# Kernel tuning notes

Hardware: AMD Instinct MI355X
Metric: run time of the kernel (lower is better)

Reference implementation:

```python
import jax, jax.numpy as jnp
import numpy as np
import math

B, T, D, H = 2, 2048, 1024, 16
DH = D // H          # 64
NB = DH // 2         # 32 rotary pairs
EPS = 1e-5


def setup_inputs() -> dict:
    key = jax.random.key(0)
    ks = jax.random.split(key, 20)
    x = jax.random.normal(ks[0], (B, T, D), dtype=jnp.float32)
    angles = jax.random.uniform(ks[1], (B, H, T, NB), dtype=jnp.float32) * (2.0 * math.pi)
    cos_a = jnp.cos(angles)
    sin_a = jnp.sin(angles)
    sigma = jax.random.uniform(ks[2], (B, T, H, NB), dtype=jnp.float32)
    causal_mask = jnp.triu(jnp.ones((T, T), dtype=bool), k=1)  # True above diag -> masked
    w = lambda k, i, o: jax.random.normal(k, (i, o), dtype=jnp.float32) * 0.02
    return {
        "x": x, "cos_a": cos_a, "sin_a": sin_a, "sigma": sigma, "causal_mask": causal_mask,
        "ln1_g": jnp.ones((D,), jnp.float32), "ln1_b": jnp.zeros((D,), jnp.float32),
        "wq": w(ks[3], D, D), "bq": jnp.zeros((D,), jnp.float32),
        "wk": w(ks[4], D, D), "bk": jnp.zeros((D,), jnp.float32),
        "wv": w(ks[5], D, D), "bv": jnp.zeros((D,), jnp.float32),
        "wo": w(ks[6], D, D), "bo": jnp.zeros((D,), jnp.float32),
        "ln2_g": jnp.ones((D,), jnp.float32), "ln2_b": jnp.zeros((D,), jnp.float32),
        "w1": w(ks[7], D, 4 * D), "b1": jnp.zeros((4 * D,), jnp.float32),
        "w2": w(ks[8], 4 * D, D), "b2": jnp.zeros((D,), jnp.float32),
    }


def _layer_norm(x, g, b):
    mu = jnp.mean(x, axis=-1, keepdims=True)
    var = jnp.mean(jnp.square(x - mu), axis=-1, keepdims=True)
    return (x - mu) * jax.lax.rsqrt(var + EPS) * g + b


def _apply_rope(q, cos_a, sin_a):
    # q: (B,H,T,DH); rotate even/odd pairs by per-pair angles (B,H,T,NB)
    q1 = q[..., 0::2]
    q2 = q[..., 1::2]
    re = q1 * cos_a - q2 * sin_a
    im = q1 * sin_a + q2 * cos_a
    return jnp.stack([re, im], axis=-1).reshape(q.shape)


def reference(x, cos_a, sin_a, sigma, causal_mask,
              ln1_g, ln1_b, wq, bq, wk, bk, wv, bv, wo, bo,
              ln2_g, ln2_b, w1, b1, w2, b2):
    h = _layer_norm(x, ln1_g, ln1_b)
    Q = (h @ wq + bq).reshape(B, T, H, DH).transpose(0, 2, 1, 3)
    K = (h @ wk + bk).reshape(B, T, H, DH).transpose(0, 2, 1, 3)
    V = (h @ wv + bv).reshape(B, T, H, DH).transpose(0, 2, 1, 3)
    Q = _apply_rope(Q, cos_a, sin_a)
    K = _apply_rope(K, cos_a, sin_a)
    # per-(B,H,T) temperature from mean uncertainty
    temp = 1.0 + jnp.mean(sigma, axis=-1).transpose(0, 2, 1)  # (B,H,T)
    scale = math.sqrt(DH)
    scores = jnp.einsum("bhtd,bhsd->bhts", Q, K) / (scale * temp[..., None])
    scores = jnp.where(causal_mask[None, None], -jnp.inf, scores)
    attn = jax.nn.softmax(scores, axis=-1)
    out = jnp.einsum("bhts,bhsd->bhtd", attn, V)
    out = out.transpose(0, 2, 1, 3).reshape(B, T, D)
    x = x + (out @ wo + bo)
    h2 = _layer_norm(x, ln2_g, ln2_b)
    ffn = jax.nn.gelu(h2 @ w1 + b1, approximate=False) @ w2 + b2
    return x + ffn
```

## Files before the change

kernel.cpp:

```cpp
#include <hip/hip_runtime.h>

typedef unsigned short ushort;
typedef unsigned int uint;

typedef __attribute__((ext_vector_type(8))) short short8;
typedef __attribute__((ext_vector_type(8))) unsigned short ushort8;
typedef __attribute__((ext_vector_type(4))) unsigned short ushort4v;
typedef __attribute__((ext_vector_type(4))) float f32x4;
typedef __attribute__((ext_vector_type(4))) uint uint4v;

#define DEV static __device__ __forceinline__

DEV ushort f2b(float f){
  union { float f; uint u; } v; v.f = f;
  uint u = v.u;
  u += 0x7fffu + ((u >> 16) & 1u);
  return (ushort)(u >> 16);
}
DEV float b2f(ushort h){
  union { uint u; float f; } v; v.u = ((uint)h) << 16;
  return v.f;
}
DEV uint cvt_pk_bf16(float lo, float hi){
  uint r;
  asm("v_cvt_pk_bf16_f32 %0, %1, %2" : "=v"(r) : "v"(lo), "v"(hi));
  return r;
}
DEV ushort f2b1(float f){ return (ushort)cvt_pk_bf16(f, f); }
DEV float exp2v(float x){
  float r;
  asm("v_exp_f32 %0, %1" : "=v"(r) : "v"(x));
  return r;
}
DEV float gelu_f(float x){
  float z = fabsf(x) * 0.70710678118654752f;
  float t = __builtin_amdgcn_rcpf(1.f + 0.3275911f * z);
  float poly = t * (0.254829592f + t * (-0.284496736f + t * (1.421413741f +
               t * (-1.453152027f + t * 1.061405429f))));
  float e = exp2v(-z * z * 1.44269504088896f);
  float erf_abs = 1.f - poly * e;
  float erf_s = copysignf(erf_abs, x);
  return 0.5f * x * (1.f + erf_s);
}

constexpr int Bc = 2, Tc = 2048, Dc = 1024, Hc = 16, DHc = 64, NBc = 32;
constexpr int Rc = Bc * Tc;
constexpr int D4c = 4 * Dc;

__global__ __launch_bounds__(256) void k_transcvt(const float* __restrict__ in,
                                                  ushort* __restrict__ out, int K, int N){
  __shared__ float tile[32][33];
  int n0 = blockIdx.x * 32, k0 = blockIdx.y * 32;
  int c = threadIdx.x & 31, r0 = threadIdx.x >> 5;
#pragma unroll
  for (int i = 0; i < 4; i++){
    int k = r0 + i * 8;
    tile[k][c] = in[(size_t)(k0 + k) * N + n0 + c];
  }
  __syncthreads();
#pragma unroll
  for (int i = 0; i < 4; i++){
    int n = r0 + i * 8;
    out[(size_t)(n0 + n) * K + k0 + c] = f2b(tile[c][n]);
  }
}

__global__ __launch_bounds__(256) void k_ln(const float* __restrict__ x, const float* __restrict__ g,
                                            const float* __restrict__ bb, ushort* __restrict__ out){
  int row = blockIdx.x, tid = threadIdx.x;
  const f32x4* xr = (const f32x4*)(x + (size_t)row * Dc);
  f32x4 v = xr[tid];
  float s  = v.x + v.y + v.z + v.w;
  float ss = v.x*v.x + v.y*v.y + v.z*v.z + v.w*v.w;
#pragma unroll
  for (int off = 32; off > 0; off >>= 1){
    s  += __shfl_xor(s,  off, 64);
    ss += __shfl_xor(ss, off, 64);
  }
  __shared__ float red[2][4];
  int w = tid >> 6;
  if ((tid & 63) == 0){ red[0][w] = s; red[1][w] = ss; }
  __syncthreads();
  s  = red[0][0] + red[0][1] + red[0][2] + red[0][3];
  ss = red[1][0] + red[1][1] + red[1][2] + red[1][3];
  float mu  = s * (1.f / Dc);
  float var = ss * (1.f / Dc) - mu * mu;
  float rs  = rsqrtf(var + 1e-5f);
  f32x4 gv = ((const f32x4*)g)[tid];
  f32x4 bv = ((const f32x4*)bb)[tid];
  ushort4v o;
  o.x = f2b((v.x - mu) * rs * gv.x + bv.x);
  o.y = f2b((v.y - mu) * rs * gv.y + bv.y);
  o.z = f2b((v.z - mu) * rs * gv.z + bv.z);
  o.w = f2b((v.w - mu) * rs * gv.w + bv.w);
  ((ushort4v*)(out + (size_t)row * Dc))[tid] = o;
}

#define GLDS(src, dst) __builtin_amdgcn_global_load_lds( \
    (const __attribute__((address_space(1))) void*)(src), \
    (__attribute__((address_space(3))) void*)(dst), 16, 0, 0)

#define STAGE128(nb_, k0_) do { \
  _Pragma("unroll") \
  for (int i_ = 0; i_ < 4; i_++){ \
    int chunk_ = w * 4 + i_; \
    GLDS(A  + (size_t)(m0 + chunk_ * 8 + rloc) * K + (k0_) + gsrc * 8, &SM[nb_][0][chunk_ * 512]); \
    GLDS(Bt + (size_t)(n0 + chunk_ * 8 + rloc) * K + (k0_) + gsrc * 8, &SM[nb_][1][chunk_ * 512]); \
  } \
} while(0)

#define GEMM_CORE(cb_) do { \
  _Pragma("unroll") \
  for (int ks = 0; ks < 2; ks++){ \
    const int gs = (ks * 4 + lg) ^ l7; \
    short8 aF[4], bF[4]; \
    _Pragma("unroll") \
    for (int mi = 0; mi < 4; mi++) aF[mi] = *(const short8*)&SM[cb_][0][(arow + mi * 16) * 64 + gs * 8]; \
    _Pragma("unroll") \
    for (int ni = 0; ni < 4; ni++) bF[ni] = *(const short8*)&SM[cb_][1][(brow + ni * 16) * 64 + gs * 8]; \
    _Pragma("unroll") \
    for (int mi = 0; mi < 4; mi++) \
      _Pragma("unroll") \
      for (int ni = 0; ni < 4; ni++) \
        acc[mi][ni] = __builtin_amdgcn_mfma_f32_16x16x32_bf16(aF[mi], bF[ni], acc[mi][ni], 0, 0, 0); \
  } \
} while(0)

template<int OUT_BF16, int ACT_GELU, int HAS_RES>
__global__ __launch_bounds__(256) void k_gemm(const ushort* __restrict__ A, const ushort* __restrict__ Bt,
                                              const float* __restrict__ bias, const float* __restrict__ resid,
                                              void* __restrict__ Cout, int M, int N, int K){
  __shared__ ushort SM[2][2][8192];
  const int tid = threadIdx.x;
  const int m0 = blockIdx.y * 128, n0 = blockIdx.x * 128;
  const int w = tid >> 6, lane = tid & 63;
  const int wr = w >> 1, wc = w & 1;
  const int la15 = lane & 15, lg = lane >> 4, l7 = lane & 7;
  const int rloc = lane >> 3, gsrc = (lane & 7) ^ rloc;

  f32x4 acc[4][4];
#pragma unroll
  for (int i = 0; i < 4; i++)
#pragma unroll
    for (int j = 0; j < 4; j++) acc[i][j] = f32x4{0.f, 0.f, 0.f, 0.f};

  const int arow = wr * 64 + la15;
  const int brow = wc * 64 + la15;

  STAGE128(0, 0);
  __syncthreads();
  const int NT = K >> 6;
  for (int t = 0; t < NT; t++){
    const int cb = t & 1;
    if (t + 1 < NT) STAGE128(cb ^ 1, (t + 1) << 6);
    GEMM_CORE(cb);
    __syncthreads();
  }

  if (OUT_BF16){
    ushort* Cs = &SM[0][0][0];
#pragma unroll
    for (int mi = 0; mi < 4; mi++)
#pragma unroll
      for (int ni = 0; ni < 4; ni++){
        int ccl = wc * 64 + ni * 16 + la15;
        float bv = bias[n0 + ccl];
        f32x4 a4 = acc[mi][ni];
#pragma unroll
        for (int r = 0; r < 4; r++){
          int rl = wr * 64 + mi * 16 + lg * 4 + r;
          float v = a4[r] + bv;
          if (ACT_GELU) v = gelu_f(v);
          Cs[rl * 136 + ccl] = f2b1(v);
        }
      }
    __syncthreads();
#pragma unroll
    for (int p = 0; p < 8; p++){
      int row = p * 16 + (tid >> 4);
      int col = (tid & 15) * 8;
      ushort8 vv = *(const ushort8*)&Cs[row * 136 + col];
      *(ushort8*)((ushort*)Cout + (size_t)(m0 + row) * N + n0 + col) = vv;
    }
  } else {
#pragma unroll
    for (int mi = 0; mi < 4; mi++)
#pragma unroll
      for (int ni = 0; ni < 4; ni++){
        int cc = n0 + wc * 64 + ni * 16 + la15;
        float bv = bias[cc];
        f32x4 a4 = acc[mi][ni];
#pragma unroll
        for (int r = 0; r < 4; r++){
          int rr = m0 + wr * 64 + mi * 16 + lg * 4 + r;
          float v = a4[r] + bv;
          if (HAS_RES) v += resid[(size_t)rr * N + cc];
          ((float*)Cout)[(size_t)rr * N + cc] = v;
        }
      }
  }
}

__global__ __launch_bounds__(256) void k_gemm_qkv(const ushort* __restrict__ A, const ushort* __restrict__ Bt,
                                                  const float* __restrict__ bq_, const float* __restrict__ bk_,
                                                  const float* __restrict__ bv_, ushort* __restrict__ oq,
                                                  ushort* __restrict__ ok, ushort* __restrict__ ovt, int K){
  __shared__ ushort SM[2][2][8192];
  const int tid = threadIdx.x;
  const int m0 = blockIdx.y * 128, n0 = blockIdx.x * 128;
  const int w = tid >> 6, lane = tid & 63;
  const int wr = w >> 1, wc = w & 1;
  const int la15 = lane & 15, lg = lane >> 4, l7 = lane & 7;
  const int rloc = lane >> 3, gsrc = (lane & 7) ^ rloc;

  f32x4 acc[4][4];
#pragma unroll
  for (int i = 0; i < 4; i++)
#pragma unroll
    for (int j = 0; j < 4; j++) acc[i][j] = f32x4{0.f, 0.f, 0.f, 0.f};

  const int arow = wr * 64 + la15;
  const int brow = wc * 64 + la15;

  STAGE128(0, 0);
  __syncthreads();
  const int NT = K >> 6;
  for (int t = 0; t < NT; t++){
    const int cb = t & 1;
    if (t + 1 < NT) STAGE128(cb ^ 1, (t + 1) << 6);
    GEMM_CORE(cb);
    __syncthreads();
  }

  const int sel = n0 >> 10;
  ushort* Cs = &SM[0][0][0];
  if (sel < 2){
    const float* bias = sel == 0 ? bq_ : bk_;
    ushort* o = sel == 0 ? oq : ok;
#pragma unroll
    for (int mi = 0; mi < 4; mi++)
#pragma unroll
      for (int ni = 0; ni < 4; ni++){
        int ccl = wc * 64 + ni * 16 + la15;
        float bv = bias[(n0 & 1023) + ccl];
        f32x4 a4 = acc[mi][ni];
#pragma unroll
        for (int r = 0; r < 4; r++){
          int rl = wr * 64 + mi * 16 + lg * 4 + r;
          Cs[rl * 136 + ccl] = f2b1(a4[r] + bv);
        }
      }
    __syncthreads();
#pragma unroll
    for (int p = 0; p < 8; p++){
      int row = p * 16 + (tid >> 4);
      int col = (tid & 15) * 8;
      ushort8 vv = *(const ushort8*)&Cs[row * 136 + col];
      *(ushort8*)(o + (size_t)(m0 + row) * Dc + (n0 & 1023) + col) = vv;
    }
  } else {
#pragma unroll
    for (int mi = 0; mi < 4; mi++)
#pragma unroll
      for (int ni = 0; ni < 4; ni++){
        int ccl = wc * 64 + ni * 16 + la15;
        float bv = bv_[(n0 - 2048) + ccl];
        f32x4 a4 = acc[mi][ni];
#pragma unroll
        for (int r = 0; r < 4; r++){
          int rl = wr * 64 + mi * 16 + lg * 4 + r;
          Cs[ccl * 136 + rl] = f2b1(a4[r] + bv);
        }
      }
    __syncthreads();
    const int bb = m0 >> 11, t0 = m0 & 2047;
#pragma unroll
    for (int p = 0; p < 8; p++){
      int nl = p * 16 + (tid >> 4);
      int tl = (tid & 15) * 8;
      ushort8 vv = *(const ushort8*)&Cs[nl * 136 + tl];
      int ng = (n0 - 2048) + nl;
      *(ushort8*)(ovt + ((size_t)(bb * 1024 + ng) << 11) + t0 + tl) = vv;
    }
  }
}

__global__ __launch_bounds__(256) void k_rope(ushort* __restrict__ q, ushort* __restrict__ k,
                                              const float* __restrict__ ca, const float* __restrict__ sa){
  int idx = blockIdx.x * 256 + threadIdx.x;
  int nb = idx & 31;
  int hh = (idx >> 5) & 15;
  int t  = (idx >> 9) & 2047;
  int b  = idx >> 20;
  size_t base = (size_t)(b * Tc + t) * Dc + hh * DHc + nb * 2;
  int ai = ((b * Hc + hh) * Tc + t) * NBc + nb;
  float c = ca[ai], s = sa[ai];
  uint qu = *(const uint*)(q + base);
  float q1 = b2f((ushort)(qu & 0xffff)), q2 = b2f((ushort)(qu >> 16));
  *(uint*)(q + base) = cvt_pk_bf16(q1 * c - q2 * s, q1 * s + q2 * c);
  uint ku = *(const uint*)(k + base);
  float k1 = b2f((ushort)(ku & 0xffff)), k2 = b2f((ushort)(ku >> 16));
  *(uint*)(k + base) = cvt_pk_bf16(k1 * c - k2 * s, k1 * s + k2 * c);
}

__global__ __launch_bounds__(256) void k_iscale(const float* __restrict__ sigma, float* __restrict__ isc){
  int idx = blockIdx.x * 256 + threadIdx.x;
  int hh = idx & 15;
  int t  = (idx >> 4) & 2047;
  int b  = idx >> 15;
  const f32x4* sp = (const f32x4*)(sigma + (size_t)idx * NBc);
  float s = 0.f;
#pragma unroll
  for (int i = 0; i < 8; i++){ f32x4 v = sp[i]; s += v.x + v.y + v.z + v.w; }
  isc[(b * Hc + hh) * Tc + t] = 1.44269504088896f / (8.f * (1.f + s * (1.f / NBc)));
}

__global__ __launch_bounds__(64) void k_attn_mfma(const ushort* __restrict__ qb, const ushort* __restrict__ kb,
                                                  const ushort* __restrict__ vtb, const float* __restrict__ isc,
                                                  ushort* __restrict__ ao){
  const int bid = blockIdx.x;
  const int bh = bid & 31, b = bh >> 4, h = bh & 15;
  const int qt = 63 - (bid >> 5);
  const int lane = threadIdx.x;
  const int la15 = lane & 15, lg = lane >> 4, l7 = lane & 7;
  const int q0w = qt * 32;
  const int kprm = ((la15 >> 2) << 3) + (la15 & 3);

  short8 qf[2][2];
  float iscv[2];
#pragma unroll
  for (int sub = 0; sub < 2; sub++){
    int qg = q0w + sub * 16 + la15;
    size_t rb = (size_t)(b * Tc + qg) * Dc + h * DHc;
    qf[sub][0] = *(const short8*)(qb + rb + lg * 8);
    qf[sub][1] = *(const short8*)(qb + rb + 32 + lg * 8);
    iscv[sub] = isc[bh * Tc + qg];
  }

  f32x4 O[2][4];
#pragma unroll
  for (int sub = 0; sub < 2; sub++)
#pragma unroll
    for (int dt = 0; dt < 4; dt++) O[sub][dt] = f32x4{0.f, 0.f, 0.f, 0.f};
  float lacc[2] = {0.f, 0.f};

  const ushort* kbase  = kb + (size_t)b * Tc * Dc + h * DHc;
  const ushort* vtbase = vtb + (size_t)bh * DHc * Tc;
  const int ktmax = q0w + 31;

#define LOADT(KF, VF, kt_) do { \
  _Pragma("unroll") \
  for (int tt_ = 0; tt_ < 4; tt_++){ \
    const ushort* kr_ = kbase + (size_t)((kt_) + kprm + ((tt_ & 1) << 2) + ((tt_ >> 1) << 5)) * Dc + lg * 8; \
    KF[tt_][0] = *(const short8*)kr_; \
    KF[tt_][1] = *(const short8*)(kr_ + 32); \
  } \
  _Pragma("unroll") \
  for (int dd_ = 0; dd_ < 4; dd_++){ \
    const ushort* vr_ = vtbase + (size_t)(dd_ * 16 + la15) * Tc + (kt_) + lg * 8; \
    VF[dd_][0] = *(const short8*)vr_; \
    VF[dd_][1] = *(const short8*)(vr_ + 32); \
  } \
} while(0)

#define COMPUTE(KF, VF, kt_) do { \
  _Pragma("unroll") \
  for (int sub = 0; sub < 2; sub++){ \
    f32x4 s_[4]; \
    _Pragma("unroll") \
    for (int t_ = 0; t_ < 4; t_++){ \
      s_[t_] = f32x4{0.f, 0.f, 0.f, 0.f}; \
      s_[t_] = __builtin_amdgcn_mfma_f32_16x16x32_bf16(KF[t_][0], qf[sub][0], s_[t_], 0, 0, 0); \
      s_[t_] = __builtin_amdgcn_mfma_f32_16x16x32_bf16(KF[t_][1], qf[sub][1], s_[t_], 0, 0, 0); \
    } \
    const int qg_ = q0w + sub * 16 + la15; \
    const float sc_ = iscv[sub]; \
    const bool diag_ = ((kt_) + 63 > q0w + sub * 16); \
    uint up_[4][2]; \
    float lp_ = 0.f; \
    _Pragma("unroll") \
    for (int t_ = 0; t_ < 4; t_++){ \
      _Pragma("unroll") \
      for (int pr_ = 0; pr_ < 2; pr_++){ \
        float e0_ = exp2v(s_[t_][2 * pr_] * sc_); \
        float e1_ = exp2v(s_[t_][2 * pr_ + 1] * sc_); \
        if (diag_){ \
          int kp0_ = (kt_) + ((t_ >> 1) << 5) + lg * 8 + ((t_ & 1) << 2) + 2 * pr_; \
          if (kp0_ > qg_)     e0_ = 0.f; \
          if (kp0_ + 1 > qg_) e1_ = 0.f; \
        } \
        lp_ += e0_ + e1_; \
        up_[t_][pr_] = cvt_pk_bf16(e0_, e1_); \
      } \
    } \
    lacc[sub] += lp_; \
    _Pragma("unroll") \
    for (int kh_ = 0; kh_ < 2; kh_++){ \
      union { uint4v w; short8 s8; } pfr_; \
      pfr_.w[0] = up_[kh_ * 2][0];     pfr_.w[1] = up_[kh_ * 2][1]; \
      pfr_.w[2] = up_[kh_ * 2 + 1][0]; pfr_.w[3] = up_[kh_ * 2 + 1][1]; \
      _Pragma("unroll") \
      for (int dt_ = 0; dt_ < 4; dt_++) \
        O[sub][dt_] = __builtin_amdgcn_mfma_f32_16x16x32_bf16(VF[dt_][kh_], pfr_.s8, O[sub][dt_], 0, 0, 0); \
    } \
  } \
} while(0)

  short8 kfA[4][2], vtfA[4][2], kfB[4][2], vtfB[4][2];
  LOADT(kfA, vtfA, 0);
  for (int kt = 0;; kt += 128){
    if (kt + 64 <= ktmax) LOADT(kfB, vtfB, kt + 64);
    COMPUTE(kfA, vtfA, kt);
    if (kt + 64 > ktmax) break;
    if (kt + 128 <= ktmax) LOADT(kfA, vtfA, kt + 128);
    COMPUTE(kfB, vtfB, kt + 64);
    if (kt + 128 > ktmax) break;
  }

  __shared__ ushort os[2176];
  char* osb = (char*)os;
#pragma unroll
  for (int sub = 0; sub < 2; sub++){
    float lt = lacc[sub];
    lt += __shfl_xor(lt, 16, 64);
    lt += __shfl_xor(lt, 32, 64);
    float inv = 1.f / lt;
#pragma unroll
    for (int dt = 0; dt < 4; dt++)
#pragma unroll
      for (int pr = 0; pr < 2; pr++){
        uint u = cvt_pk_bf16(O[sub][dt][2 * pr] * inv, O[sub][dt][2 * pr + 1] * inv);
        *(uint*)(osb + (sub * 16 + la15) * 136 + (dt * 16 + lg * 4 + pr * 2) * 2) = u;
      }
  }
#pragma unroll
  for (int it = 0; it < 4; it++){
    int ql = it * 8 + (lane >> 3);
    ushort8 v = *(const ushort8*)(osb + ql * 136 + l7 * 16);
    *(ushort8*)(ao + (size_t)(b * Tc + q0w + ql) * Dc + h * DHc + l7 * 8) = v;
  }
}

extern "C" void kernel_launch(void* const* d_in, const int* in_sizes, int n_in,
                              void* d_out, int out_size, void* d_ws, size_t ws_size,
                              hipStream_t stream){
  (void)in_sizes; (void)n_in; (void)out_size; (void)ws_size;
  const float* x    = (const float*)d_in[0];
  const float* cosa = (const float*)d_in[1];
  const float* sina = (const float*)d_in[2];
  const float* sigma= (const float*)d_in[3];
  const float* ln1g = (const float*)d_in[5];
  const float* ln1b = (const float*)d_in[6];
  const float* wq   = (const float*)d_in[7];
  const float* bq   = (const float*)d_in[8];
  const float* wk   = (const float*)d_in[9];
  const float* bk   = (const float*)d_in[10];
  const float* wv   = (const float*)d_in[11];
  const float* bv   = (const float*)d_in[12];
  const float* wo   = (const float*)d_in[13];
  const float* bo   = (const float*)d_in[14];
  const float* ln2g = (const float*)d_in[15];
  const float* ln2b = (const float*)d_in[16];
  const float* w1   = (const float*)d_in[17];
  const float* b1   = (const float*)d_in[18];
  const float* w2   = (const float*)d_in[19];
  const float* b2   = (const float*)d_in[20];
  float* out = (float*)d_out;

  char* ws = (char*)d_ws;
  constexpr size_t MB = 1024 * 1024;
  ushort* wqT  = (ushort*)(ws +  0 * MB);
  ushort* wkT  = (ushort*)(ws +  2 * MB);
  ushort* wvT  = (ushort*)(ws +  4 * MB);
  ushort* woT  = (ushort*)(ws +  6 * MB);
  ushort* w1T  = (ushort*)(ws +  8 * MB);
  ushort* w2T  = (ushort*)(ws + 16 * MB);
  ushort* hb   = (ushort*)(ws + 24 * MB);
  ushort* qbuf = (ushort*)(ws + 32 * MB);
  ushort* kbuf = (ushort*)(ws + 40 * MB);
  ushort* vtb  = (ushort*)(ws + 48 * MB);
  ushort* aob  = (ushort*)(ws + 56 * MB);
  float*  x2   = (float*)(ws + 64 * MB);
  float*  iscp = (float*)(ws + 80 * MB);
  ushort* g1b  = qbuf;

  k_transcvt<<<dim3(Dc / 32, Dc / 32), 256, 0, stream>>>(wq, wqT, Dc, Dc);
  k_transcvt<<<dim3(Dc / 32, Dc / 32), 256, 0, stream>>>(wk, wkT, Dc, Dc);
  k_transcvt<<<dim3(Dc / 32, Dc / 32), 256, 0, stream>>>(wv, wvT, Dc, Dc);
  k_transcvt<<<dim3(Dc / 32, Dc / 32), 256, 0, stream>>>(wo, woT, Dc, Dc);
  k_transcvt<<<dim3(D4c / 32, Dc / 32), 256, 0, stream>>>(w1, w1T, Dc, D4c);
  k_transcvt<<<dim3(Dc / 32, D4c / 32), 256, 0, stream>>>(w2, w2T, D4c, Dc);
  k_ln<<<Rc, 256, 0, stream>>>(x, ln1g, ln1b, hb);
  k_gemm_qkv<<<dim3(3 * Dc / 128, Rc / 128), 256, 0, stream>>>(hb, wqT, bq, bk, bv, qbuf, kbuf, vtb, Dc);
  k_rope<<<(Bc * Tc * Hc * NBc) / 256, 256, 0, stream>>>(qbuf, kbuf, cosa, sina);
  k_iscale<<<(Bc * Tc * Hc) / 256, 256, 0, stream>>>(sigma, iscp);
  k_attn_mfma<<<dim3(2048), 64, 0, stream>>>(qbuf, kbuf, vtb, iscp, aob);
  k_gemm<0, 0, 1><<<dim3(Dc / 128, Rc / 128), 256, 0, stream>>>(aob, woT, bo, x, x2, Rc, Dc, Dc);
  k_ln<<<Rc, 256, 0, stream>>>(x2, ln2g, ln2b, hb);
  k_gemm<1, 1, 0><<<dim3(D4c / 128, Rc / 128), 256, 0, stream>>>(hb, w1T, b1, nullptr, g1b, Rc, D4c, Dc);
  k_gemm<0, 0, 1><<<dim3(Dc / 128, Rc / 128), 256, 0, stream>>>(g1b, w2T, b2, x2, out, Rc, Dc, D4c);
}
```

Baseline: 265.1 us.

## Use a four-stage LDS ring pipeline in GEMMs and prefetch deeper in attention

The GEMM main loop moves from a two-buffer, 64-wide K step to a four-slot LDS ring with a 32-wide K step. Three stages stay in flight, gated by explicit vmcnt waits and raw barriers, and a new XOR swizzle matches the narrower tiles. MFMA blocks in both the GEMM and attention kernels are wrapped in s_setprio so matrix work gets issue priority. The attention loop now prefetches the next K/V tile unconditionally, and its launch bounds change to (64, 1). Both kernels now issue speculative loads past the valid K range, which risks out-of-bounds reads on the final iterations.

```diff
diff --git a/kernel.cpp b/kernel.cpp
--- a/kernel.cpp
+++ b/kernel.cpp
@@ -100,43 +100,63 @@
     (const __attribute__((address_space(1))) void*)(src), \
     (__attribute__((address_space(3))) void*)(dst), 16, 0, 0)
 
-#define STAGE128(nb_, k0_) do { \
+#define STAGE_R(ring_, k0_) do { \
+  GLDS(A  + (size_t)(m0 + grow)      * K + (k0_) + g4 * 8, &SM[ring_][0][w * 512]); \
+  GLDS(A  + (size_t)(m0 + 64 + grow) * K + (k0_) + g4 * 8, &SM[ring_][0][2048 + w * 512]); \
+  GLDS(Bt + (size_t)(n0 + grow)      * K + (k0_) + g4 * 8, &SM[ring_][1][w * 512]); \
+  GLDS(Bt + (size_t)(n0 + 64 + grow) * K + (k0_) + g4 * 8, &SM[ring_][1][2048 + w * 512]); \
+} while(0)
+
+#define CORE_R(cb_) do { \
+  const ushort* As_ = &SM[cb_][0][0]; \
+  const ushort* Bs_ = &SM[cb_][1][0]; \
+  short8 aF[4], bF[4]; \
   _Pragma("unroll") \
-  for (int i_ = 0; i_ < 4; i_++){ \
-    int chunk_ = w * 4 + i_; \
-    GLDS(A  + (size_t)(m0 + chunk_ * 8 + rloc) * K + (k0_) + gsrc * 8, &SM[nb_][0][chunk_ * 512]); \
-    GLDS(Bt + (size_t)(n0 + chunk_ * 8 + rloc) * K + (k0_) + gsrc * 8, &SM[nb_][1][chunk_ * 512]); \
+  for (int mi = 0; mi < 4; mi++){ \
+    int r_ = arow + mi * 16; \
+    aF[mi] = *(const short8*)&As_[r_ * 32 + (lg ^ ((r_ >> 1) & 3)) * 8]; \
   } \
+  _Pragma("unroll") \
+  for (int ni = 0; ni < 4; ni++){ \
+    int r_ = brow + ni * 16; \
+    bF[ni] = *(const short8*)&Bs_[r_ * 32 + (lg ^ ((r_ >> 1) & 3)) * 8]; \
+  } \
+  __builtin_amdgcn_s_setprio(1); \
+  _Pragma("unroll") \
+  for (int mi = 0; mi < 4; mi++) \
+    _Pragma("unroll") \
+    for (int ni = 0; ni < 4; ni++) \
+      acc[mi][ni] = __builtin_amdgcn_mfma_f32_16x16x32_bf16(aF[mi], bF[ni], acc[mi][ni], 0, 0, 0); \
+  __builtin_amdgcn_s_setprio(0); \
 } while(0)
 
-#define GEMM_CORE(cb_) do { \
-  _Pragma("unroll") \
-  for (int ks = 0; ks < 2; ks++){ \
-    const int gs = (ks * 4 + lg) ^ l7; \
-    short8 aF[4], bF[4]; \
-    _Pragma("unroll") \
-    for (int mi = 0; mi < 4; mi++) aF[mi] = *(const short8*)&SM[cb_][0][(arow + mi * 16) * 64 + gs * 8]; \
-    _Pragma("unroll") \
-    for (int ni = 0; ni < 4; ni++) bF[ni] = *(const short8*)&SM[cb_][1][(brow + ni * 16) * 64 + gs * 8]; \
-    _Pragma("unroll") \
-    for (int mi = 0; mi < 4; mi++) \
-      _Pragma("unroll") \
-      for (int ni = 0; ni < 4; ni++) \
-        acc[mi][ni] = __builtin_amdgcn_mfma_f32_16x16x32_bf16(aF[mi], bF[ni], acc[mi][ni], 0, 0, 0); \
+#define RING_LOOP() do { \
+  STAGE_R(0, 0); STAGE_R(1, 32); STAGE_R(2, 64); \
+  asm volatile("s_waitcnt vmcnt(8)" ::: "memory"); \
+  __builtin_amdgcn_s_barrier(); \
+  const int NT_ = K >> 5; \
+  for (int t = 0; t < NT_; t++){ \
+    STAGE_R((t + 3) & 3, (t + 3) << 5); \
+    CORE_R(t & 3); \
+    asm volatile("s_waitcnt vmcnt(8)" ::: "memory"); \
+    __builtin_amdgcn_s_barrier(); \
   } \
+  asm volatile("s_waitcnt vmcnt(0)" ::: "memory"); \
+  __builtin_amdgcn_s_barrier(); \
 } while(0)
 
 template<int OUT_BF16, int ACT_GELU, int HAS_RES>
 __global__ __launch_bounds__(256) void k_gemm(const ushort* __restrict__ A, const ushort* __restrict__ Bt,
                                               const float* __restrict__ bias, const float* __restrict__ resid,
                                               void* __restrict__ Cout, int M, int N, int K){
-  __shared__ ushort SM[2][2][8192];
+  __shared__ ushort SM[4][2][4096];
   const int tid = threadIdx.x;
   const int m0 = blockIdx.y * 128, n0 = blockIdx.x * 128;
   const int w = tid >> 6, lane = tid & 63;
   const int wr = w >> 1, wc = w & 1;
-  const int la15 = lane & 15, lg = lane >> 4, l7 = lane & 7;
-  const int rloc = lane >> 3, gsrc = (lane & 7) ^ rloc;
+  const int la15 = lane & 15, lg = lane >> 4;
+  const int grow = w * 16 + (lane >> 2);
+  const int g4 = (lane & 3) ^ ((lane >> 3) & 3);
 
   f32x4 acc[4][4];
 #pragma unroll
@@ -147,18 +167,10 @@
   const int arow = wr * 64 + la15;
   const int brow = wc * 64 + la15;
 
-  STAGE128(0, 0);
-  __syncthreads();
-  const int NT = K >> 6;
-  for (int t = 0; t < NT; t++){
-    const int cb = t & 1;
-    if (t + 1 < NT) STAGE128(cb ^ 1, (t + 1) << 6);
-    GEMM_CORE(cb);
-    __syncthreads();
-  }
+  RING_LOOP();
 
   if (OUT_BF16){
-    ushort* Cs = &SM[0][0][0];
+    ushort* Cs = (ushort*)SM;
 #pragma unroll
     for (int mi = 0; mi < 4; mi++)
 #pragma unroll
@@ -168,7 +180,7 @@
         f32x4 a4 = acc[mi][ni];
 #pragma unroll
         for (int r = 0; r < 4; r++){
-          int rl = wr * 64 + mi * 16 + lg * 4 + r;
+          int rl = wr * 64 + mi * 16 + (lane >> 4) * 4 + r;
           float v = a4[r] + bv;
           if (ACT_GELU) v = gelu_f(v);
           Cs[rl * 136 + ccl] = f2b1(v);
@@ -192,7 +204,7 @@
         f32x4 a4 = acc[mi][ni];
 #pragma unroll
         for (int r = 0; r < 4; r++){
-          int rr = m0 + wr * 64 + mi * 16 + lg * 4 + r;
+          int rr = m0 + wr * 64 + mi * 16 + (lane >> 4) * 4 + r;
           float v = a4[r] + bv;
           if (HAS_RES) v += resid[(size_t)rr * N + cc];
           ((float*)Cout)[(size_t)rr * N + cc] = v;
@@ -205,13 +217,14 @@
                                                   const float* __restrict__ bq_, const float* __restrict__ bk_,
                                                   const float* __restrict__ bv_, ushort* __restrict__ oq,
                                                   ushort* __restrict__ ok, ushort* __restrict__ ovt, int K){
-  __shared__ ushort SM[2][2][8192];
+  __shared__ ushort SM[4][2][4096];
   const int tid = threadIdx.x;
   const int m0 = blockIdx.y * 128, n0 = blockIdx.x * 128;
   const int w = tid >> 6, lane = tid & 63;
   const int wr = w >> 1, wc = w & 1;
-  const int la15 = lane & 15, lg = lane >> 4, l7 = lane & 7;
-  const int rloc = lane >> 3, gsrc = (lane & 7) ^ rloc;
+  const int la15 = lane & 15, lg = lane >> 4;
+  const int grow = w * 16 + (lane >> 2);
+  const int g4 = (lane & 3) ^ ((lane >> 3) & 3);
 
   f32x4 acc[4][4];
 #pragma unroll
@@ -222,18 +235,10 @@
   const int arow = wr * 64 + la15;
   const int brow = wc * 64 + la15;
 
-  STAGE128(0, 0);
-  __syncthreads();
-  const int NT = K >> 6;
-  for (int t = 0; t < NT; t++){
-    const int cb = t & 1;
-    if (t + 1 < NT) STAGE128(cb ^ 1, (t + 1) << 6);
-    GEMM_CORE(cb);
-    __syncthreads();
-  }
+  RING_LOOP();
 
   const int sel = n0 >> 10;
-  ushort* Cs = &SM[0][0][0];
+  ushort* Cs = (ushort*)SM;
   if (sel < 2){
     const float* bias = sel == 0 ? bq_ : bk_;
     ushort* o = sel == 0 ? oq : ok;
@@ -246,7 +251,7 @@
         f32x4 a4 = acc[mi][ni];
 #pragma unroll
         for (int r = 0; r < 4; r++){
-          int rl = wr * 64 + mi * 16 + lg * 4 + r;
+          int rl = wr * 64 + mi * 16 + (lane >> 4) * 4 + r;
           Cs[rl * 136 + ccl] = f2b1(a4[r] + bv);
         }
       }
@@ -268,7 +273,7 @@
         f32x4 a4 = acc[mi][ni];
 #pragma unroll
         for (int r = 0; r < 4; r++){
-          int rl = wr * 64 + mi * 16 + lg * 4 + r;
+          int rl = wr * 64 + mi * 16 + (lane >> 4) * 4 + r;
           Cs[ccl * 136 + rl] = f2b1(a4[r] + bv);
         }
       }
@@ -315,9 +320,9 @@
   isc[(b * Hc + hh) * Tc + t] = 1.44269504088896f / (8.f * (1.f + s * (1.f / NBc)));
 }
 
-__global__ __launch_bounds__(64) void k_attn_mfma(const ushort* __restrict__ qb, const ushort* __restrict__ kb,
-                                                  const ushort* __restrict__ vtb, const float* __restrict__ isc,
-                                                  ushort* __restrict__ ao){
+__global__ __launch_bounds__(64, 1) void k_attn_mfma(const ushort* __restrict__ qb, const ushort* __restrict__ kb,
+                                                     const ushort* __restrict__ vtb, const float* __restrict__ isc,
+                                                     ushort* __restrict__ ao){
   const int bid = blockIdx.x;
   const int bh = bid & 31, b = bh >> 4, h = bh & 15;
   const int qt = 63 - (bid >> 5);
@@ -367,12 +372,14 @@
   _Pragma("unroll") \
   for (int sub = 0; sub < 2; sub++){ \
     f32x4 s_[4]; \
+    __builtin_amdgcn_s_setprio(1); \
     _Pragma("unroll") \
     for (int t_ = 0; t_ < 4; t_++){ \
       s_[t_] = f32x4{0.f, 0.f, 0.f, 0.f}; \
       s_[t_] = __builtin_amdgcn_mfma_f32_16x16x32_bf16(KF[t_][0], qf[sub][0], s_[t_], 0, 0, 0); \
       s_[t_] = __builtin_amdgcn_mfma_f32_16x16x32_bf16(KF[t_][1], qf[sub][1], s_[t_], 0, 0, 0); \
     } \
+    __builtin_amdgcn_s_setprio(0); \
     const int qg_ = q0w + sub * 16 + la15; \
     const float sc_ = iscv[sub]; \
     const bool diag_ = ((kt_) + 63 > q0w + sub * 16); \
@@ -394,6 +401,7 @@
       } \
     } \
     lacc[sub] += lp_; \
+    __builtin_amdgcn_s_setprio(1); \
     _Pragma("unroll") \
     for (int kh_ = 0; kh_ < 2; kh_++){ \
       union { uint4v w; short8 s8; } pfr_; \
@@ -403,18 +411,20 @@
       for (int dt_ = 0; dt_ < 4; dt_++) \
         O[sub][dt_] = __builtin_amdgcn_mfma_f32_16x16x32_bf16(VF[dt_][kh_], pfr_.s8, O[sub][dt_], 0, 0, 0); \
     } \
+    __builtin_amdgcn_s_setprio(0); \
   } \
 } while(0)
 
   short8 kfA[4][2], vtfA[4][2], kfB[4][2], vtfB[4][2];
   LOADT(kfA, vtfA, 0);
+  LOADT(kfB, vtfB, 64);
   for (int kt = 0;; kt += 128){
-    if (kt + 64 <= ktmax) LOADT(kfB, vtfB, kt + 64);
     COMPUTE(kfA, vtfA, kt);
     if (kt + 64 > ktmax) break;
-    if (kt + 128 <= ktmax) LOADT(kfA, vtfA, kt + 128);
+    LOADT(kfA, vtfA, kt + 128);
     COMPUTE(kfB, vtfB, kt + 64);
     if (kt + 128 > ktmax) break;
+    LOADT(kfB, vtfB, kt + 192);
   }
 
   __shared__ ushort os[2176];
```

Result: slower. 273.9 us (+3.3%).

## Stage attention K/V tiles through swizzled LDS with async global-to-LDS loads

Applied to the files above, without the earlier changes.

The attention kernel no longer double-buffers K and V^T fragments in registers with direct global loads. Each 64-key tile is now copied into shared memory with global-to-LDS loads using an XOR swizzle, then read back into MFMA fragments. The load of the next tile is issued while the current one is computed. The MFMA sections are also wrapped in s_setprio to raise wave priority. This aims to coalesce global traffic and free registers, at the cost of extra LDS round trips and explicit waitcnt stalls. The last iteration also prefetches a tile past the causal range, which may read out of bounds.

```diff
diff --git a/kernel.cpp b/kernel.cpp
--- a/kernel.cpp
+++ b/kernel.cpp
@@ -318,13 +318,13 @@
 __global__ __launch_bounds__(64) void k_attn_mfma(const ushort* __restrict__ qb, const ushort* __restrict__ kb,
                                                   const ushort* __restrict__ vtb, const float* __restrict__ isc,
                                                   ushort* __restrict__ ao){
+  __shared__ ushort smem[8192];
   const int bid = blockIdx.x;
   const int bh = bid & 31, b = bh >> 4, h = bh & 15;
   const int qt = 63 - (bid >> 5);
   const int lane = threadIdx.x;
   const int la15 = lane & 15, lg = lane >> 4, l7 = lane & 7;
   const int q0w = qt * 32;
-  const int kprm = ((la15 >> 2) << 3) + (la15 & 3);
 
   short8 qf[2][2];
   float iscv[2];
@@ -348,31 +348,32 @@
   const ushort* vtbase = vtb + (size_t)bh * DHc * Tc;
   const int ktmax = q0w + 31;
 
-#define LOADT(KF, VF, kt_) do { \
+  const int Rl = lane >> 3, sl = lane & 7;
+  const int gK = sl ^ ((Rl & 3) ^ (((Rl >> 3) & 3) << 1));
+  const int gV = sl ^ (Rl & 7);
+
+#define STAGE_KV(kt_) do { \
   _Pragma("unroll") \
-  for (int tt_ = 0; tt_ < 4; tt_++){ \
-    const ushort* kr_ = kbase + (size_t)((kt_) + kprm + ((tt_ & 1) << 2) + ((tt_ >> 1) << 5)) * Dc + lg * 8; \
-    KF[tt_][0] = *(const short8*)kr_; \
-    KF[tt_][1] = *(const short8*)(kr_ + 32); \
-  } \
-  _Pragma("unroll") \
-  for (int dd_ = 0; dd_ < 4; dd_++){ \
-    const ushort* vr_ = vtbase + (size_t)(dd_ * 16 + la15) * Tc + (kt_) + lg * 8; \
-    VF[dd_][0] = *(const short8*)vr_; \
-    VF[dd_][1] = *(const short8*)(vr_ + 32); \
+  for (int i_ = 0; i_ < 8; i_++){ \
+    int R_ = i_ * 8 + Rl; \
+    int gk_ = sl ^ ((R_ & 3) ^ (((R_ >> 3) & 3) << 1)); \
+    GLDS(kbase + (size_t)((kt_) + R_) * Dc + gk_ * 8, &smem[i_ * 512]); \
+    GLDS(vtbase + (size_t)R_ * Tc + (kt_) + gV * 8, &smem[4096 + i_ * 512]); \
   } \
 } while(0)
 
-#define COMPUTE(KF, VF, kt_) do { \
+#define COMPUTE_T(kt_) do { \
   _Pragma("unroll") \
   for (int sub = 0; sub < 2; sub++){ \
     f32x4 s_[4]; \
+    __builtin_amdgcn_s_setprio(1); \
     _Pragma("unroll") \
     for (int t_ = 0; t_ < 4; t_++){ \
       s_[t_] = f32x4{0.f, 0.f, 0.f, 0.f}; \
-      s_[t_] = __builtin_amdgcn_mfma_f32_16x16x32_bf16(KF[t_][0], qf[sub][0], s_[t_], 0, 0, 0); \
-      s_[t_] = __builtin_amdgcn_mfma_f32_16x16x32_bf16(KF[t_][1], qf[sub][1], s_[t_], 0, 0, 0); \
+      s_[t_] = __builtin_amdgcn_mfma_f32_16x16x32_bf16(kf[t_][0], qf[sub][0], s_[t_], 0, 0, 0); \
+      s_[t_] = __builtin_amdgcn_mfma_f32_16x16x32_bf16(kf[t_][1], qf[sub][1], s_[t_], 0, 0, 0); \
     } \
+    __builtin_amdgcn_s_setprio(0); \
     const int qg_ = q0w + sub * 16 + la15; \
     const float sc_ = iscv[sub]; \
     const bool diag_ = ((kt_) + 63 > q0w + sub * 16); \
@@ -394,6 +395,7 @@
       } \
     } \
     lacc[sub] += lp_; \
+    __builtin_amdgcn_s_setprio(1); \
     _Pragma("unroll") \
     for (int kh_ = 0; kh_ < 2; kh_++){ \
       union { uint4v w; short8 s8; } pfr_; \
@@ -401,24 +403,49 @@
       pfr_.w[2] = up_[kh_ * 2 + 1][0]; pfr_.w[3] = up_[kh_ * 2 + 1][1]; \
       _Pragma("unroll") \
       for (int dt_ = 0; dt_ < 4; dt_++) \
-        O[sub][dt_] = __builtin_amdgcn_mfma_f32_16x16x32_bf16(VF[dt_][kh_], pfr_.s8, O[sub][dt_], 0, 0, 0); \
+        O[sub][dt_] = __builtin_amdgcn_mfma_f32_16x16x32_bf16(vtf[dt_][kh_], pfr_.s8, O[sub][dt_], 0, 0, 0); \
     } \
+    __builtin_amdgcn_s_setprio(0); \
   } \
 } while(0)
 
-  short8 kfA[4][2], vtfA[4][2], kfB[4][2], vtfB[4][2];
-  LOADT(kfA, vtfA, 0);
-  for (int kt = 0;; kt += 128){
-    if (kt + 64 <= ktmax) LOADT(kfB, vtfB, kt + 64);
-    COMPUTE(kfA, vtfA, kt);
+  STAGE_KV(0);
+  asm volatile("s_waitcnt vmcnt(0)" ::: "memory");
+  __builtin_amdgcn_sched_barrier(0);
+
+  const int swzr = (la15 & 3) ^ ((la15 >> 2) << 1);
+  for (int kt = 0;; kt += 64){
+    short8 kf[4][2], vtf[4][2];
+#pragma unroll
+    for (int t_ = 0; t_ < 4; t_++){
+      int r = ((t_ >> 1) << 5) + ((la15 >> 2) << 3) + ((t_ & 1) << 2) + (la15 & 3);
+#pragma unroll
+      for (int ds = 0; ds < 2; ds++){
+        int g = (ds * 4 + lg) ^ swzr;
+        kf[t_][ds] = *(const short8*)&smem[r * 64 + g * 8];
+      }
+    }
+#pragma unroll
+    for (int dt = 0; dt < 4; dt++){
+      int d = dt * 16 + la15;
+#pragma unroll
+      for (int kh = 0; kh < 2; kh++){
+        int g = (kh * 4 + lg) ^ (la15 & 7);
+        vtf[dt][kh] = *(const short8*)&smem[4096 + d * 64 + g * 8];
+      }
+    }
+    asm volatile("s_waitcnt lgkmcnt(0)" ::: "memory");
+    __builtin_amdgcn_sched_barrier(0);
+    STAGE_KV(kt + 64);
+    COMPUTE_T(kt);
     if (kt + 64 > ktmax) break;
-    if (kt + 128 <= ktmax) LOADT(kfA, vtfA, kt + 128);
-    COMPUTE(kfB, vtfB, kt + 64);
-    if (kt + 128 > ktmax) break;
-  }
-
-  __shared__ ushort os[2176];
-  char* osb = (char*)os;
+    asm volatile("s_waitcnt vmcnt(0)" ::: "memory");
+    __builtin_amdgcn_sched_barrier(0);
+  }
+  asm volatile("s_waitcnt vmcnt(0)" ::: "memory");
+  __builtin_amdgcn_sched_barrier(0);
+
+  char* osb = (char*)smem;
 #pragma unroll
   for (int sub = 0; sub < 2; sub++){
     float lt = lacc[sub];
```

Measured after the change: 248.1 us. -6.4%, faster.
